# Kernel tuning notes

Measured on AMD Instinct MI355X. Metric: run time of the kernel, lower is better.

## Reference

```python
import jax, jax.numpy as jnp
import numpy as np

ALPHA = 2.0   # spikingjelly surrogate.ATan default alpha
TAU = 2.0
VTH = 1.0
EPS = 1e-5

@jax.custom_vjp
def atan_spike(x):
    return (x >= 0.0).astype(x.dtype)

def _as_fwd(x):
    return atan_spike(x), x

def _as_bwd(x, g):
    # ATan surrogate derivative: alpha/2 / (1 + (pi/2*alpha*x)^2)
    return (g * (ALPHA / 2.0) / (1.0 + (jnp.pi / 2.0 * ALPHA * x) ** 2),)

atan_spike.defvjp(_as_fwd, _as_bwd)

def lif_multistep(x):
    # x: [B, T, D]; LIF with decay_input=True, v_reset=0 (hard reset), detach_reset=True
    xt = jnp.swapaxes(x, 0, 1)  # [T, B, D] time-major
    def step(v, xi):
        v = v + (xi - v) / TAU                       # integrate with input decay
        s = atan_spike(v - VTH)                       # fire (surrogate grad)
        v = v * (1.0 - jax.lax.stop_gradient(s))      # hard reset to 0, detached
        return v, s
    _, spikes = jax.lax.scan(step, jnp.zeros_like(xt[0]), xt)
    return jnp.swapaxes(spikes, 0, 1)  # [B, T, D]

def layernorm(x, g, b):
    m = x.mean(-1, keepdims=True)
    v = x.var(-1, keepdims=True)
    return (x - m) / jnp.sqrt(v + EPS) * g + b

def setup_inputs() -> dict:
    key = jax.random.key(0)
    ks = jax.random.split(key, 6)
    B, T, IN, HP, E, H, D = 256, 256, 4, 64, 512, 1024, 4
    s = 0.02
    return {
        "hist_feat": jax.random.normal(ks[0], (B, T, IN), jnp.float32),
        "pW1": jax.random.normal(ks[1], (IN, HP), jnp.float32) * s,
        "pb1": jnp.zeros((HP,), jnp.float32),
        "pW2": jax.random.normal(ks[2], (HP, E), jnp.float32) * s,
        "pb2": jnp.zeros((E,), jnp.float32),
        "fc1_w": jax.random.normal(ks[3], (D, E, H), jnp.float32) * s,
        "fc1_b": jnp.zeros((D, H), jnp.float32),
        "ln1_g": jnp.ones((D, H), jnp.float32),
        "ln1_b": jnp.zeros((D, H), jnp.float32),
        "fc2_w": jax.random.normal(ks[4], (D, H, E), jnp.float32) * s,
        "fc2_b": jnp.zeros((D, E), jnp.float32),
        "ln2_g": jnp.ones((D, E), jnp.float32),
        "ln2_b": jnp.zeros((D, E), jnp.float32),
    }

def reference(hist_feat, pW1, pb1, pW2, pb2, fc1_w, fc1_b, ln1_g, ln1_b,
              fc2_w, fc2_b, ln2_g, ln2_b):
    # input projector: Linear -> exact GELU -> Linear
    x = jax.nn.gelu(hist_feat @ pW1 + pb1, approximate=False) @ pW2 + pb2  # [B,T,E]
    depth = fc1_w.shape[0]
    for d in range(depth):  # small fixed layer loop
        res = x
        h = layernorm(x @ fc1_w[d] + fc1_b[d], ln1_g[d], ln1_b[d])  # [B,T,H]
        h = lif_multistep(h)
        h = layernorm(h @ fc2_w[d] + fc2_b[d], ln2_g[d], ln2_b[d])  # [B,T,E]
        h = lif_multistep(h)
        x = res + h  # dropout is identity in eval mode
    return x[:, -1]  # pooling='last', no mask -> last timestep, [B,E]
```

## Files before the change

### kernel.cpp

```cpp
#include <hip/hip_runtime.h>
#include <hip/hip_bf16.h>
#include <math.h>

#define B_  256
#define T_  256
#define IN_ 4
#define HP_ 64
#define E_  512
#define H_  1024
#define D_  4

typedef __hip_bfloat16 bf16;
typedef _Float16 f16;
typedef _Float16 f16x8 __attribute__((ext_vector_type(8)));
typedef float f32x4 __attribute__((ext_vector_type(4)));

__device__ __forceinline__ float load1(const void* p, size_t idx, bool isb) {
    if (isb) {
        unsigned int u = ((const unsigned short*)p)[idx];
        return __uint_as_float(u << 16);
    }
    return ((const float*)p)[idx];
}

__device__ __forceinline__ float4 load4(const void* p, size_t idx, bool isb) {
    if (isb) {
        ushort4 u = *(const ushort4*)((const unsigned short*)p + idx);
        float4 r;
        r.x = __uint_as_float(((unsigned int)u.x) << 16);
        r.y = __uint_as_float(((unsigned int)u.y) << 16);
        r.z = __uint_as_float(((unsigned int)u.z) << 16);
        r.w = __uint_as_float(((unsigned int)u.w) << 16);
        return r;
    }
    return *((const float4*)p + (idx >> 2));
}

__device__ __forceinline__ void split3(float x, f16& h, f16& hs, f16& lb) {
    h = (f16)x;
    float hf = (float)h;
    hs = (f16)(hf * 4.8828125e-4f);
    lb = (f16)((x - hf) * 2048.0f);
}

__global__ void sniff_kernel(const unsigned short* __restrict__ p,
                             int* __restrict__ flag) {
    __shared__ int cnt;
    if (threadIdx.x == 0) cnt = 0;
    __syncthreads();
    int local = 0;
    for (int i = threadIdx.x; i < 65536; i += blockDim.x) {
        unsigned int bits = ((unsigned int)p[i]) << 16;
        float v = __uint_as_float(bits);
        float a = fabsf(v);
        if (!(a <= 1e4f)) local++;
        else if (v != 0.0f && a < 1e-6f) local++;
    }
    atomicAdd(&cnt, local);
    __syncthreads();
    if (threadIdx.x == 0) *flag = (cnt > 1024) ? 0 : 1;
}

__global__ __launch_bounds__(256) void wsplit_kernel(
        const void* __restrict__ W, size_t wOff, unsigned short* __restrict__ Wt,
        int K, int N, const int* __restrict__ flag) {
    const bool isb = (*flag != 0);
    __shared__ float tile[32][33];
    const int n0 = blockIdx.x * 32, k0 = blockIdx.y * 32;
    const int t = threadIdx.x;
    {
        int lk = t >> 3, ln0 = (t & 7) << 2;
        float4 v = load4(W, wOff + (size_t)(k0 + lk) * N + n0 + ln0, isb);
        tile[lk][ln0 + 0] = v.x; tile[lk][ln0 + 1] = v.y;
        tile[lk][ln0 + 2] = v.z; tile[lk][ln0 + 3] = v.w;
    }
    __syncthreads();
    int n = t >> 3, kq0 = (t & 7) << 2;
    size_t base = (size_t)(n0 + n) * (2 * (size_t)K) + k0 + kq0;
    #pragma unroll
    for (int j = 0; j < 4; ++j) {
        float x = tile[kq0 + j][n];
        f16 h, hs, lb;
        split3(x, h, hs, lb);
        Wt[base + j]     = *(unsigned short*)&h;
        Wt[base + j + K] = *(unsigned short*)&lb;
    }
}

template<int NPL>
__device__ __forceinline__ void gemm_mfma_body(
        const unsigned short* __restrict__ At, const unsigned short* __restrict__ Wt,
        const void* __restrict__ bias, size_t bOff,
        float* __restrict__ C, int N, int K, const int* __restrict__ flag) {
    const bool isb = (*flag != 0);
    constexpr int APL = (NPL == 3) ? 2 : 1;
    __shared__ unsigned short As[128 * 64];
    __shared__ unsigned short Bs[128 * 64];

    const int gx = N >> 7;
    const int gy = (int)gridDim.x / gx;
    int bx, by;
    {
        int bid = blockIdx.x;
        if ((gy & 7) == 0) {
            int k = bid & 7, i = bid >> 3;
            bx = i % gx;
            by = (gy >> 3) * k + i / gx;
        } else { bx = bid % gx; by = bid / gx; }
    }
    const int bn = bx * 128;
    const int bm = by * 128;

    const int tid  = threadIdx.x;
    const int lane = tid & 63;
    const int wave = tid >> 6;
    const int wm = wave >> 1;
    const int wn = wave & 1;
    const int g  = lane >> 4;
    const int lr = lane & 15;

    const int sar = tid >> 1;
    const int sah = tid & 1;
    const int sbn = tid >> 1;
    const int sq  = tid & 1;

    const f16 C11 = (f16)4.8828125e-4f;
    const f16x8 c11v = {C11, C11, C11, C11, C11, C11, C11, C11};

    f32x4 acc[4][4];
    #pragma unroll
    for (int i = 0; i < 4; ++i)
        #pragma unroll
        for (int j = 0; j < 4; ++j) acc[i][j] = (f32x4){0.f, 0.f, 0.f, 0.f};

    const unsigned short* Ap = At + (size_t)(bm + sar) * (APL * (size_t)K) + sah * 16;
    const unsigned short* Wp = Wt + (size_t)(bn + sbn) * (2 * (size_t)K) + sq * 16;

    f16x8 av[2 * APL], wv[4];
    #pragma unroll
    for (int pl = 0; pl < APL; ++pl)
        #pragma unroll
        for (int c = 0; c < 2; ++c)
            av[pl * 2 + c] = *(const f16x8*)(Ap + (size_t)pl * K + c * 8);
    #pragma unroll
    for (int pl = 0; pl < 2; ++pl)
        #pragma unroll
        for (int c = 0; c < 2; ++c)
            wv[pl * 2 + c] = *(const f16x8*)(Wp + (size_t)pl * K + c * 8);

    const int nt = K >> 5;
    for (int t = 0; t < nt; ++t) {
        const int arb = sar * 64, asw = sar & 7;
        #pragma unroll
        for (int pl = 0; pl < APL; ++pl)
            #pragma unroll
            for (int c = 0; c < 2; ++c) {
                const int gg = sah * 2 + c;
                *(f16x8*)&As[arb + (((pl << 2) | gg) ^ asw) * 8] = av[pl * 2 + c];
            }
        const int brb = sbn * 64, bsw = sbn & 7;
        #pragma unroll
        for (int pl = 0; pl < 2; ++pl)
            #pragma unroll
            for (int c = 0; c < 2; ++c) {
                const int gg = sq * 2 + c;
                *(f16x8*)&Bs[brb + (((pl << 2) | gg) ^ bsw) * 8] = wv[pl * 2 + c];
            }
        __syncthreads();
        if (t + 1 < nt) {
            const int k0 = (t + 1) << 5;
            #pragma unroll
            for (int pl = 0; pl < APL; ++pl)
                #pragma unroll
                for (int c = 0; c < 2; ++c)
                    av[pl * 2 + c] = *(const f16x8*)(Ap + (size_t)pl * K + k0 + c * 8);
            #pragma unroll
            for (int pl = 0; pl < 2; ++pl)
                #pragma unroll
                for (int c = 0; c < 2; ++c)
                    wv[pl * 2 + c] = *(const f16x8*)(Wp + (size_t)pl * K + k0 + c * 8);
        }
        f16x8 a0[4], b0[4], b2[4], a2[4];
        #pragma unroll
        for (int mi = 0; mi < 4; ++mi) {
            const int ar = wm * 64 + mi * 16 + lr;
            a0[mi] = *(const f16x8*)&As[ar * 64 + ((g ^ (ar & 7))) * 8];
            if (NPL == 3)
                a2[mi] = *(const f16x8*)&As[ar * 64 + (((4 | g) ^ (ar & 7))) * 8];
        }
        #pragma unroll
        for (int ni = 0; ni < 4; ++ni) {
            const int br = wn * 64 + ni * 16 + lr;
            b0[ni] = *(const f16x8*)&Bs[br * 64 + ((g ^ (br & 7))) * 8];
            b2[ni] = *(const f16x8*)&Bs[br * 64 + (((4 | g) ^ (br & 7))) * 8];
        }
        #pragma unroll
        for (int mi = 0; mi < 4; ++mi)
            #pragma unroll
            for (int ni = 0; ni < 4; ++ni)
                acc[mi][ni] = __builtin_amdgcn_mfma_f32_16x16x32_f16(
                    a0[mi], b0[ni], acc[mi][ni], 0, 0, 0);
        {
            f16x8 a1[4];
            #pragma unroll
            for (int mi = 0; mi < 4; ++mi) a1[mi] = a0[mi] * c11v;
            #pragma unroll
            for (int mi = 0; mi < 4; ++mi)
                #pragma unroll
                for (int ni = 0; ni < 4; ++ni)
                    acc[mi][ni] = __builtin_amdgcn_mfma_f32_16x16x32_f16(
                        a1[mi], b2[ni], acc[mi][ni], 0, 0, 0);
        }
        if (NPL == 3) {
            f16x8 b1[4];
            #pragma unroll
            for (int ni = 0; ni < 4; ++ni) b1[ni] = b0[ni] * c11v;
            #pragma unroll
            for (int mi = 0; mi < 4; ++mi)
                #pragma unroll
                for (int ni = 0; ni < 4; ++ni)
                    acc[mi][ni] = __builtin_amdgcn_mfma_f32_16x16x32_f16(
                        a2[mi], b1[ni], acc[mi][ni], 0, 0, 0);
        }
        __syncthreads();
    }
    #pragma unroll
    for (int ni = 0; ni < 4; ++ni) {
        const int col = bn + wn * 64 + ni * 16 + lr;
        const float bv = load1(bias, bOff + col, isb);
        #pragma unroll
        for (int mi = 0; mi < 4; ++mi) {
            #pragma unroll
            for (int r = 0; r < 4; ++r) {
                const size_t row = (size_t)(bm + wm * 64 + mi * 16 + g * 4 + r);
                C[row * N + col] = acc[mi][ni][r] + bv;
            }
        }
    }
}

__global__ __launch_bounds__(256, 3) void gemm_mfma3_kernel(
        const unsigned short* __restrict__ At, const unsigned short* __restrict__ Wt,
        const void* __restrict__ bias, size_t bOff,
        float* __restrict__ C, int N, int K, const int* __restrict__ flag) {
    gemm_mfma_body<3>(At, Wt, bias, bOff, C, N, K, flag);
}

__global__ __launch_bounds__(256, 3) void gemm_mfma2_kernel(
        const unsigned short* __restrict__ At, const unsigned short* __restrict__ Wt,
        const void* __restrict__ bias, size_t bOff,
        float* __restrict__ C, int N, int K, const int* __restrict__ flag) {
    gemm_mfma_body<2>(At, Wt, bias, bOff, C, N, K, flag);
}

#define RB_ 16
__global__ __launch_bounds__(256) void proj_kernel(
        const void* __restrict__ hist, const void* __restrict__ pW1,
        const void* __restrict__ pb1,  const void* __restrict__ pW2,
        const void* __restrict__ pb2,  float* __restrict__ Xc,
        unsigned short* __restrict__ At1,
        size_t m0, const int* __restrict__ flag) {
    const bool isb = (*flag != 0);
    __shared__ float h1[RB_][HP_];
    const size_t mb = (size_t)blockIdx.x * RB_;
    const int tid = threadIdx.x;
    const int lane = tid & 63;
    const int grp = tid >> 6;
    #pragma unroll
    for (int rep = 0; rep < 4; ++rep) {
        int idx = tid + rep * 256;
        int r = idx >> 6, c = idx & 63;
        size_t gm = m0 + mb + r;
        float acc = 0.f;
        #pragma unroll
        for (int i = 0; i < IN_; ++i)
            acc = fmaf(load1(hist, gm * IN_ + i, isb),
                       load1(pW1, (size_t)i * HP_ + c, isb), acc);
        acc += load1(pb1, c, isb);
        h1[r][c] = 0.5f * acc * (1.0f + erff(acc * 0.70710678118654752440f));
    }
    __syncthreads();
    const int e0 = lane * 8;
    float acc[4][8];
    #pragma unroll
    for (int r = 0; r < 4; ++r)
        #pragma unroll
        for (int j = 0; j < 8; ++j) acc[r][j] = 0.f;
    for (int i = 0; i < HP_; ++i) {
        float4 wA = load4(pW2, (size_t)i * E_ + e0, isb);
        float4 wB = load4(pW2, (size_t)i * E_ + e0 + 4, isb);
        float w[8] = {wA.x, wA.y, wA.z, wA.w, wB.x, wB.y, wB.z, wB.w};
        #pragma unroll
        for (int r = 0; r < 4; ++r) {
            float h = h1[grp * 4 + r][i];
            #pragma unroll
            for (int j = 0; j < 8; ++j) acc[r][j] = fmaf(h, w[j], acc[r][j]);
        }
    }
    #pragma unroll
    for (int r = 0; r < 4; ++r) {
        size_t row = mb + grp * 4 + r;
        float o[8];
        #pragma unroll
        for (int j = 0; j < 8; ++j)
            o[j] = acc[r][j] + load1(pb2, e0 + j, isb);
        *(float4*)(Xc + row * E_ + e0)     = (float4){o[0], o[1], o[2], o[3]};
        *(float4*)(Xc + row * E_ + e0 + 4) = (float4){o[4], o[5], o[6], o[7]};
        f16x8 hv, lv;
        #pragma unroll
        for (int j = 0; j < 8; ++j) {
            f16 h, hs, lb;
            split3(o[j], h, hs, lb);
            hv[j] = h; lv[j] = lb;
        }
        *(f16x8*)&At1[row * (2 * E_) + e0]      = hv;
        *(f16x8*)&At1[row * (2 * E_) + E_ + e0] = lv;
    }
}

__device__ __forceinline__ float block_sum(float v, float* smem, int tid) {
    #pragma unroll
    for (int off = 32; off > 0; off >>= 1) v += __shfl_down(v, off, 64);
    __syncthreads();
    if ((tid & 63) == 0) smem[tid >> 6] = v;
    __syncthreads();
    if (tid == 0) smem[4] = smem[0] + smem[1] + smem[2] + smem[3];
    __syncthreads();
    return smem[4];
}

__global__ __launch_bounds__(256) void ln_stats_kernel(const float* __restrict__ Y,
                                                       float* __restrict__ stats,
                                                       int N) {
    __shared__ float smem[5];
    size_t row = blockIdx.x;
    const float* y = Y + row * (size_t)N;
    int tid = threadIdx.x;
    int nPer = N >> 8;
    float vals[4];
    float s = 0.f;
    for (int i = 0; i < nPer; ++i) { float v = y[tid + (i << 8)]; vals[i] = v; s += v; }
    float mean = block_sum(s, smem, tid) / (float)N;
    float sq = 0.f;
    for (int i = 0; i < nPer; ++i) { float d0 = vals[i] - mean; sq += d0 * d0; }
    float var = block_sum(sq, smem, tid) / (float)N;
    if (tid == 0) {
        stats[row * 2]     = mean;
        stats[row * 2 + 1] = sqrtf(var + 1e-5f);
    }
}

__global__ __launch_bounds__(64) void lif_kernel(const float* __restrict__ Y,
                                                 const float* __restrict__ stats,
                                                 const void* __restrict__ g, size_t gOff,
                                                 const void* __restrict__ b, size_t bOff,
                                                 unsigned short* __restrict__ At2,
                                                 int N, const int* __restrict__ flag) {
    const bool isb = (*flag != 0);
    int f = blockIdx.x * 64 + threadIdx.x;
    int bb = blockIdx.y;
    const float gw = load1(g, gOff + f, isb);
    const float bw = load1(b, bOff + f, isb);
    size_t base = (size_t)bb * T_ * N + f;
    size_t srow = (size_t)bb * T_;
    float v = 0.f;
    for (int t0 = 0; t0 < T_; t0 += 8) {
        float x[8], mn[8], dn[8], s[8];
        #pragma unroll
        for (int j = 0; j < 8; ++j) {
            x[j]  = Y[base + (size_t)(t0 + j) * N];
            mn[j] = stats[(srow + t0 + j) * 2];
            dn[j] = stats[(srow + t0 + j) * 2 + 1];
        }
        #pragma unroll
        for (int j = 0; j < 8; ++j) {
            float xn = (x[j] - mn[j]) / dn[j] * gw + bw;
            v = v + (xn - v) * 0.5f;
            s[j] = (v - 1.0f >= 0.0f) ? 1.0f : 0.0f;
            v = v * (1.0f - s[j]);
        }
        #pragma unroll
        for (int j = 0; j < 8; ++j) {
            f16 h = (f16)s[j];
            At2[base + (size_t)(t0 + j) * N] = *(unsigned short*)&h;
        }
    }
}

__global__ __launch_bounds__(64) void lif_add_kernel(const float* __restrict__ Z,
                                                     const float* __restrict__ stats,
                                                     const void* __restrict__ g, size_t gOff,
                                                     const void* __restrict__ b, size_t bOff,
                                                     float* __restrict__ Xc,
                                                     unsigned short* __restrict__ At1,
                                                     const int* __restrict__ flag) {
    const bool isb = (*flag != 0);
    int e = blockIdx.x * 64 + threadIdx.x;
    int bb = blockIdx.y;
    const float gw = load1(g, gOff + e, isb);
    const float bw = load1(b, bOff + e, isb);
    size_t base  = (size_t)bb * T_ * E_ + e;
    size_t base2 = (size_t)bb * T_ * (2 * E_) + e;
    size_t srow  = (size_t)bb * T_;
    float v = 0.f;
    for (int t0 = 0; t0 < T_; t0 += 8) {
        float x[8], xc[8], mn[8], dn[8], s[8];
        #pragma unroll
        for (int j = 0; j < 8; ++j) {
            x[j]  = Z[base + (size_t)(t0 + j) * E_];
            mn[j] = stats[(srow + t0 + j) * 2];
            dn[j] = stats[(srow + t0 + j) * 2 + 1];
        }
        #pragma unroll
        for (int j = 0; j < 8; ++j) xc[j] = Xc[base + (size_t)(t0 + j) * E_];
        #pragma unroll
        for (int j = 0; j < 8; ++j) {
            float xn = (x[j] - mn[j]) / dn[j] * gw + bw;
            v = v + (xn - v) * 0.5f;
            s[j] = (v - 1.0f >= 0.0f) ? 1.0f : 0.0f;
            v = v * (1.0f - s[j]);
        }
        #pragma unroll
        for (int j = 0; j < 8; ++j) {
            float nx = xc[j] + s[j];
            Xc[base + (size_t)(t0 + j) * E_] = nx;
            f16 h, hs, lb;
            split3(nx, h, hs, lb);
            At1[base2 + (size_t)(t0 + j) * (2 * E_)]      = *(unsigned short*)&h;
            At1[base2 + (size_t)(t0 + j) * (2 * E_) + E_] = *(unsigned short*)&lb;
        }
    }
}

__global__ void out_kernel(const float* __restrict__ Xc, void* __restrict__ out,
                           int b0, const int* __restrict__ flag) {
    int i = blockIdx.x * 256 + threadIdx.x;
    int bl = i / E_, e = i - bl * E_;
    float v = Xc[((size_t)bl * T_ + (T_ - 1)) * E_ + e];
    size_t oi = (size_t)(b0 + bl) * E_ + e;
    if (*flag) ((bf16*)out)[oi] = __float2bfloat16(v);
    else       ((float*)out)[oi] = v;
}

extern "C" void kernel_launch(void* const* d_in, const int* in_sizes, int n_in,
                              void* d_out, int out_size, void* d_ws, size_t ws_size,
                              hipStream_t stream) {
    char* ws = (char*)d_ws;
    int* flag = (int*)ws;

    const size_t wtCount = 2 * (size_t)E_ * H_;
    const size_t wtBytes = 2 * D_ * wtCount * sizeof(unsigned short);
    unsigned short* Wt1 = (unsigned short*)(ws + 256);
    unsigned short* Wt2 = Wt1 + (size_t)D_ * wtCount;

    size_t used = 256 + wtBytes;
    size_t avail = (ws_size > used) ? ws_size - used : 0;
    const size_t perBatch = (size_t)T_ * ((E_ + H_ + E_) * 4 + 2 * E_ * 2 + H_ * 2 + 16);
    int CB = 256;
    while (CB > 1 && (size_t)CB * perBatch > avail) CB >>= 1;
    const int R = CB * T_;

    float* Xc  = (float*)(ws + used);
    float* HBc = Xc + (size_t)R * E_;
    float* Y2c = HBc + (size_t)R * H_;
    unsigned short* At1 = (unsigned short*)(Y2c + (size_t)R * E_);
    unsigned short* At2 = At1 + (size_t)R * 2 * E_;
    float* St1 = (float*)(At2 + (size_t)R * H_);
    float* St2 = St1 + (size_t)R * 2;

    sniff_kernel<<<1, 256, 0, stream>>>((const unsigned short*)d_in[0], flag);

    for (int d = 0; d < D_; ++d) {
        wsplit_kernel<<<dim3(H_ / 32, E_ / 32), 256, 0, stream>>>(
            d_in[5], (size_t)d * E_ * H_, Wt1 + (size_t)d * wtCount, E_, H_, flag);
        wsplit_kernel<<<dim3(E_ / 32, H_ / 32), 256, 0, stream>>>(
            d_in[9], (size_t)d * H_ * E_, Wt2 + (size_t)d * wtCount, H_, E_, flag);
    }

    for (int b0 = 0; b0 < B_; b0 += CB) {
        proj_kernel<<<R / RB_, 256, 0, stream>>>(d_in[0], d_in[1], d_in[2], d_in[3],
                                                 d_in[4], Xc, At1, (size_t)b0 * T_, flag);
        for (int d = 0; d < D_; ++d) {
            size_t b1o = (size_t)d * H_;
            size_t b2o = (size_t)d * E_;

            gemm_mfma3_kernel<<<(H_ / 128) * (R / 128), 256, 0, stream>>>(
                At1, Wt1 + (size_t)d * wtCount, d_in[6], b1o, HBc, H_, E_, flag);
            ln_stats_kernel<<<R, 256, 0, stream>>>(HBc, St1, H_);
            lif_kernel<<<dim3(H_ / 64, CB), 64, 0, stream>>>(
                HBc, St1, d_in[7], b1o, d_in[8], b1o, At2, H_, flag);

            gemm_mfma2_kernel<<<(E_ / 128) * (R / 128), 256, 0, stream>>>(
                At2, Wt2 + (size_t)d * wtCount, d_in[10], b2o, Y2c, E_, H_, flag);
            ln_stats_kernel<<<R, 256, 0, stream>>>(Y2c, St2, E_);
            lif_add_kernel<<<dim3(E_ / 64, CB), 64, 0, stream>>>(
                Y2c, St2, d_in[11], b2o, d_in[12], b2o, Xc, At1, flag);
        }
        out_kernel<<<(CB * E_) / 256, 256, 0, stream>>>(Xc, d_out, b0, flag);
    }
}
```

Measured before the change: 3.503 ms.

## Specialise GEMM kernels, shrink fc2 tile to 64 rows, parallelise dtype sniff, alias buffers

The templated GEMM body is split into two dedicated kernels. The fc2 GEMM now uses a 64x128 tile with half the threads staging A, which doubles its grid. Occupancy hints change to 4 and 5 blocks per CU. The dtype sniff now runs across 64 blocks plus a tiny reduction kernel, and Y2c aliases HBc so the per-batch workspace shrinks and a larger chunk can fit. The smaller tile raises parallelism and occupancy but lowers reuse of W per block. The aliasing depends on HBc being dead by the time the second GEMM writes.

```diff
diff --git a/kernel.cpp b/kernel.cpp
--- a/kernel.cpp
+++ b/kernel.cpp
@@ -43,13 +43,15 @@
     lb = (f16)((x - hf) * 2048.0f);
 }
 
-__global__ void sniff_kernel(const unsigned short* __restrict__ p,
-                             int* __restrict__ flag) {
+__global__ void sniff_count_kernel(const unsigned short* __restrict__ p,
+                                   int* __restrict__ cnts) {
     __shared__ int cnt;
     if (threadIdx.x == 0) cnt = 0;
     __syncthreads();
     int local = 0;
-    for (int i = threadIdx.x; i < 65536; i += blockDim.x) {
+    #pragma unroll
+    for (int k = 0; k < 4; ++k) {
+        int i = blockIdx.x * 1024 + k * 256 + threadIdx.x;
         unsigned int bits = ((unsigned int)p[i]) << 16;
         float v = __uint_as_float(bits);
         float a = fabsf(v);
@@ -58,7 +60,14 @@
     }
     atomicAdd(&cnt, local);
     __syncthreads();
-    if (threadIdx.x == 0) *flag = (cnt > 1024) ? 0 : 1;
+    if (threadIdx.x == 0) cnts[blockIdx.x] = cnt;
+}
+
+__global__ void sniff_final_kernel(const int* __restrict__ cnts,
+                                   int* __restrict__ flag) {
+    int s = 0;
+    for (int i = 0; i < 64; ++i) s += cnts[i];
+    *flag = (s > 1024) ? 0 : 1;
 }
 
 __global__ __launch_bounds__(256) void wsplit_kernel(
@@ -87,13 +96,11 @@
     }
 }
 
-template<int NPL>
-__device__ __forceinline__ void gemm_mfma_body(
+__global__ __launch_bounds__(256, 4) void gemm_mfma3_kernel(
         const unsigned short* __restrict__ At, const unsigned short* __restrict__ Wt,
         const void* __restrict__ bias, size_t bOff,
         float* __restrict__ C, int N, int K, const int* __restrict__ flag) {
     const bool isb = (*flag != 0);
-    constexpr int APL = (NPL == 3) ? 2 : 1;
     __shared__ unsigned short As[128 * 64];
     __shared__ unsigned short Bs[128 * 64];
 
@@ -133,60 +140,48 @@
         #pragma unroll
         for (int j = 0; j < 4; ++j) acc[i][j] = (f32x4){0.f, 0.f, 0.f, 0.f};
 
-    const unsigned short* Ap = At + (size_t)(bm + sar) * (APL * (size_t)K) + sah * 16;
+    const unsigned short* Ap = At + (size_t)(bm + sar) * (2 * (size_t)K) + sah * 16;
     const unsigned short* Wp = Wt + (size_t)(bn + sbn) * (2 * (size_t)K) + sq * 16;
 
-    f16x8 av[2 * APL], wv[4];
-    #pragma unroll
-    for (int pl = 0; pl < APL; ++pl)
-        #pragma unroll
-        for (int c = 0; c < 2; ++c)
+    f16x8 av[4], wv[4];
+    #pragma unroll
+    for (int pl = 0; pl < 2; ++pl)
+        #pragma unroll
+        for (int c = 0; c < 2; ++c) {
             av[pl * 2 + c] = *(const f16x8*)(Ap + (size_t)pl * K + c * 8);
-    #pragma unroll
-    for (int pl = 0; pl < 2; ++pl)
-        #pragma unroll
-        for (int c = 0; c < 2; ++c)
             wv[pl * 2 + c] = *(const f16x8*)(Wp + (size_t)pl * K + c * 8);
+        }
 
     const int nt = K >> 5;
     for (int t = 0; t < nt; ++t) {
         const int arb = sar * 64, asw = sar & 7;
-        #pragma unroll
-        for (int pl = 0; pl < APL; ++pl)
+        const int brb = sbn * 64, bsw = sbn & 7;
+        #pragma unroll
+        for (int pl = 0; pl < 2; ++pl)
             #pragma unroll
             for (int c = 0; c < 2; ++c) {
                 const int gg = sah * 2 + c;
                 *(f16x8*)&As[arb + (((pl << 2) | gg) ^ asw) * 8] = av[pl * 2 + c];
-            }
-        const int brb = sbn * 64, bsw = sbn & 7;
-        #pragma unroll
-        for (int pl = 0; pl < 2; ++pl)
-            #pragma unroll
-            for (int c = 0; c < 2; ++c) {
-                const int gg = sq * 2 + c;
-                *(f16x8*)&Bs[brb + (((pl << 2) | gg) ^ bsw) * 8] = wv[pl * 2 + c];
+                const int gb = sq * 2 + c;
+                *(f16x8*)&Bs[brb + (((pl << 2) | gb) ^ bsw) * 8] = wv[pl * 2 + c];
             }
         __syncthreads();
         if (t + 1 < nt) {
             const int k0 = (t + 1) << 5;
             #pragma unroll
-            for (int pl = 0; pl < APL; ++pl)
-                #pragma unroll
-                for (int c = 0; c < 2; ++c)
-                    av[pl * 2 + c] = *(const f16x8*)(Ap + (size_t)pl * K + k0 + c * 8);
-            #pragma unroll
             for (int pl = 0; pl < 2; ++pl)
                 #pragma unroll
-                for (int c = 0; c < 2; ++c)
+                for (int c = 0; c < 2; ++c) {
+                    av[pl * 2 + c] = *(const f16x8*)(Ap + (size_t)pl * K + k0 + c * 8);
                     wv[pl * 2 + c] = *(const f16x8*)(Wp + (size_t)pl * K + k0 + c * 8);
+                }
         }
         f16x8 a0[4], b0[4], b2[4], a2[4];
         #pragma unroll
         for (int mi = 0; mi < 4; ++mi) {
             const int ar = wm * 64 + mi * 16 + lr;
             a0[mi] = *(const f16x8*)&As[ar * 64 + ((g ^ (ar & 7))) * 8];
-            if (NPL == 3)
-                a2[mi] = *(const f16x8*)&As[ar * 64 + (((4 | g) ^ (ar & 7))) * 8];
+            a2[mi] = *(const f16x8*)&As[ar * 64 + (((4 | g) ^ (ar & 7))) * 8];
         }
         #pragma unroll
         for (int ni = 0; ni < 4; ++ni) {
@@ -211,7 +206,7 @@
                     acc[mi][ni] = __builtin_amdgcn_mfma_f32_16x16x32_f16(
                         a1[mi], b2[ni], acc[mi][ni], 0, 0, 0);
         }
-        if (NPL == 3) {
+        {
             f16x8 b1[4];
             #pragma unroll
             for (int ni = 0; ni < 4; ++ni) b1[ni] = b0[ni] * c11v;
@@ -239,18 +234,142 @@
     }
 }
 
-__global__ __launch_bounds__(256, 3) void gemm_mfma3_kernel(
+__global__ __launch_bounds__(256, 5) void gemm_mfma2_kernel(
         const unsigned short* __restrict__ At, const unsigned short* __restrict__ Wt,
         const void* __restrict__ bias, size_t bOff,
         float* __restrict__ C, int N, int K, const int* __restrict__ flag) {
-    gemm_mfma_body<3>(At, Wt, bias, bOff, C, N, K, flag);
-}
-
-__global__ __launch_bounds__(256, 3) void gemm_mfma2_kernel(
-        const unsigned short* __restrict__ At, const unsigned short* __restrict__ Wt,
-        const void* __restrict__ bias, size_t bOff,
-        float* __restrict__ C, int N, int K, const int* __restrict__ flag) {
-    gemm_mfma_body<2>(At, Wt, bias, bOff, C, N, K, flag);
+    const bool isb = (*flag != 0);
+    __shared__ unsigned short As[64 * 64];
+    __shared__ unsigned short Bs[128 * 64];
+
+    const int gx = N >> 7;
+    const int gy = (int)gridDim.x / gx;
+    int bx, by;
+    {
+        int bid = blockIdx.x;
+        if ((gy & 7) == 0) {
+            int k = bid & 7, i = bid >> 3;
+            bx = i % gx;
+            by = (gy >> 3) * k + i / gx;
+        } else { bx = bid % gx; by = bid / gx; }
+    }
+    const int bn = bx * 128;
+    const int bm = by * 64;
+
+    const int tid  = threadIdx.x;
+    const int lane = tid & 63;
+    const int wave = tid >> 6;
+    const int wm = wave >> 1;
+    const int wn = wave & 1;
+    const int g  = lane >> 4;
+    const int lr = lane & 15;
+
+    const int sar = (tid >> 1) & 63;
+    const int sah = tid & 1;
+    const int sbn = tid >> 1;
+    const int sq  = tid & 1;
+    const bool aStage = (tid < 128);
+
+    const f16 C11 = (f16)4.8828125e-4f;
+    const f16x8 c11v = {C11, C11, C11, C11, C11, C11, C11, C11};
+
+    f32x4 acc[2][4];
+    #pragma unroll
+    for (int i = 0; i < 2; ++i)
+        #pragma unroll
+        for (int j = 0; j < 4; ++j) acc[i][j] = (f32x4){0.f, 0.f, 0.f, 0.f};
+
+    const unsigned short* Ap = At + (size_t)(bm + sar) * (size_t)K + sah * 16;
+    const unsigned short* Wp = Wt + (size_t)(bn + sbn) * (2 * (size_t)K) + sq * 16;
+
+    f16x8 av[2], wv[4];
+    if (aStage) {
+        av[0] = *(const f16x8*)(Ap);
+        av[1] = *(const f16x8*)(Ap + 8);
+    }
+    #pragma unroll
+    for (int pl = 0; pl < 2; ++pl)
+        #pragma unroll
+        for (int c = 0; c < 2; ++c)
+            wv[pl * 2 + c] = *(const f16x8*)(Wp + (size_t)pl * K + c * 8);
+
+    const int nt = K >> 5;
+    for (int t = 0; t < nt; ++t) {
+        if (aStage) {
+            const int arb = sar * 64, asw = sar & 7;
+            #pragma unroll
+            for (int c = 0; c < 2; ++c) {
+                const int gg = sah * 2 + c;
+                *(f16x8*)&As[arb + ((gg ^ asw)) * 8] = av[c];
+            }
+        }
+        {
+            const int brb = sbn * 64, bsw = sbn & 7;
+            #pragma unroll
+            for (int pl = 0; pl < 2; ++pl)
+                #pragma unroll
+                for (int c = 0; c < 2; ++c) {
+                    const int gb = sq * 2 + c;
+                    *(f16x8*)&Bs[brb + (((pl << 2) | gb) ^ bsw) * 8] = wv[pl * 2 + c];
+                }
+        }
+        __syncthreads();
+        if (t + 1 < nt) {
+            const int k0 = (t + 1) << 5;
+            if (aStage) {
+                av[0] = *(const f16x8*)(Ap + k0);
+                av[1] = *(const f16x8*)(Ap + k0 + 8);
+            }
+            #pragma unroll
+            for (int pl = 0; pl < 2; ++pl)
+                #pragma unroll
+                for (int c = 0; c < 2; ++c)
+                    wv[pl * 2 + c] = *(const f16x8*)(Wp + (size_t)pl * K + k0 + c * 8);
+        }
+        f16x8 a0[2], b0[4], b2[4];
+        #pragma unroll
+        for (int mi = 0; mi < 2; ++mi) {
+            const int ar = wm * 32 + mi * 16 + lr;
+            a0[mi] = *(const f16x8*)&As[ar * 64 + ((g ^ (ar & 7))) * 8];
+        }
+        #pragma unroll
+        for (int ni = 0; ni < 4; ++ni) {
+            const int br = wn * 64 + ni * 16 + lr;
+            b0[ni] = *(const f16x8*)&Bs[br * 64 + ((g ^ (br & 7))) * 8];
+            b2[ni] = *(const f16x8*)&Bs[br * 64 + (((4 | g) ^ (br & 7))) * 8];
+        }
+        #pragma unroll
+        for (int mi = 0; mi < 2; ++mi)
+            #pragma unroll
+            for (int ni = 0; ni < 4; ++ni)
+                acc[mi][ni] = __builtin_amdgcn_mfma_f32_16x16x32_f16(
+                    a0[mi], b0[ni], acc[mi][ni], 0, 0, 0);
+        {
+            f16x8 a1[2];
+            #pragma unroll
+            for (int mi = 0; mi < 2; ++mi) a1[mi] = a0[mi] * c11v;
+            #pragma unroll
+            for (int mi = 0; mi < 2; ++mi)
+                #pragma unroll
+                for (int ni = 0; ni < 4; ++ni)
+                    acc[mi][ni] = __builtin_amdgcn_mfma_f32_16x16x32_f16(
+                        a1[mi], b2[ni], acc[mi][ni], 0, 0, 0);
+        }
+        __syncthreads();
+    }
+    #pragma unroll
+    for (int ni = 0; ni < 4; ++ni) {
+        const int col = bn + wn * 64 + ni * 16 + lr;
+        const float bv = load1(bias, bOff + col, isb);
+        #pragma unroll
+        for (int mi = 0; mi < 2; ++mi) {
+            #pragma unroll
+            for (int r = 0; r < 4; ++r) {
+                const size_t row = (size_t)(bm + wm * 32 + mi * 16 + g * 4 + r);
+                C[row * N + col] = acc[mi][ni][r] + bv;
+            }
+        }
+    }
 }
 
 #define RB_ 16
@@ -447,28 +566,30 @@
                               hipStream_t stream) {
     char* ws = (char*)d_ws;
     int* flag = (int*)ws;
+    int* cnts = (int*)(ws + 64);
 
     const size_t wtCount = 2 * (size_t)E_ * H_;
     const size_t wtBytes = 2 * D_ * wtCount * sizeof(unsigned short);
-    unsigned short* Wt1 = (unsigned short*)(ws + 256);
+    unsigned short* Wt1 = (unsigned short*)(ws + 512);
     unsigned short* Wt2 = Wt1 + (size_t)D_ * wtCount;
 
-    size_t used = 256 + wtBytes;
+    size_t used = 512 + wtBytes;
     size_t avail = (ws_size > used) ? ws_size - used : 0;
-    const size_t perBatch = (size_t)T_ * ((E_ + H_ + E_) * 4 + 2 * E_ * 2 + H_ * 2 + 16);
+    const size_t perBatch = (size_t)T_ * (E_ * 4 + H_ * 4 + 2 * E_ * 2 + H_ * 2 + 16);
     int CB = 256;
     while (CB > 1 && (size_t)CB * perBatch > avail) CB >>= 1;
     const int R = CB * T_;
 
     float* Xc  = (float*)(ws + used);
     float* HBc = Xc + (size_t)R * E_;
-    float* Y2c = HBc + (size_t)R * H_;
-    unsigned short* At1 = (unsigned short*)(Y2c + (size_t)R * E_);
+    float* Y2c = HBc;
+    unsigned short* At1 = (unsigned short*)(HBc + (size_t)R * H_);
     unsigned short* At2 = At1 + (size_t)R * 2 * E_;
     float* St1 = (float*)(At2 + (size_t)R * H_);
     float* St2 = St1 + (size_t)R * 2;
 
-    sniff_kernel<<<1, 256, 0, stream>>>((const unsigned short*)d_in[0], flag);
+    sniff_count_kernel<<<64, 256, 0, stream>>>((const unsigned short*)d_in[0], cnts);
+    sniff_final_kernel<<<1, 1, 0, stream>>>(cnts, flag);
 
     for (int d = 0; d < D_; ++d) {
         wsplit_kernel<<<dim3(H_ / 32, E_ / 32), 256, 0, stream>>>(
@@ -490,7 +611,7 @@
             lif_kernel<<<dim3(H_ / 64, CB), 64, 0, stream>>>(
                 HBc, St1, d_in[7], b1o, d_in[8], b1o, At2, H_, flag);
 
-            gemm_mfma2_kernel<<<(E_ / 128) * (R / 128), 256, 0, stream>>>(
+            gemm_mfma2_kernel<<<(E_ / 128) * (R / 64), 256, 0, stream>>>(
                 At2, Wt2 + (size_t)d * wtCount, d_in[10], b2o, Y2c, E_, H_, flag);
             ln_stats_kernel<<<R, 256, 0, stream>>>(Y2c, St2, E_);
             lif_add_kernel<<<dim3(E_ / 64, CB), 64, 0, stream>>>(
```

Result: slower. 6.439 ms (+83.8%).
